# Optimization experiments

Hardware: AMD Instinct MI355X
Metric: run time of the kernel (lower is better)

Reference implementation:

```python
import jax, jax.numpy as jnp
import numpy as np
from jax.scipy.special import logsumexp

B, N1, N2, D = 32, 512, 512, 128
M_WARP = 256   # n_warp_fn_times
M_DISCR = 96   # n_warp_discr (warp-value grid per time step)
GAMMA = 0.1    # softmin temperature (soft relaxation of the hard-argmin GDTW DP)
BARRIER = 1e4  # soft penalty enforcing endpoint + local-gradient constraints


def setup_inputs() -> dict:
    key = jax.random.key(0)
    k1, k2, k3 = jax.random.split(key, 3)
    return {
        "signal1_features": jax.random.normal(k1, (B, N1, D), jnp.float32),
        "signal2_features": jax.random.normal(k2, (B, N2, D), jnp.float32),
        "reg_wt": jax.random.uniform(k3, (B,), jnp.float32, 0.1, 1.0),
        "glb_lb": jnp.zeros((B, M_WARP), jnp.float32),
        "glb_ub": jnp.ones((B, M_WARP), jnp.float32),
        "lcl_grad_ub": 2.0 * jnp.ones((B, 1), jnp.float32),
        "signal1_times": jnp.broadcast_to(jnp.linspace(0.0, 1.0, N1, dtype=jnp.float32)[None], (B, N1)),
        "signal2_times": jnp.broadcast_to(jnp.linspace(0.0, 1.0, N2, dtype=jnp.float32)[None], (B, N2)),
        "warp_fn_times": jnp.broadcast_to(jnp.linspace(0.0, 1.0, M_WARP, dtype=jnp.float32)[None], (B, M_WARP)),
    }


def _interp_uniform(feats, pos):
    """Linear interpolation of feats [b,n,d] at normalized positions pos in [0,1]."""
    b, n, d = feats.shape
    shp = pos.shape
    x = jnp.clip(pos, 0.0, 1.0) * (n - 1)
    i0 = jnp.clip(x.astype(jnp.int32), 0, n - 2)
    w = (x - i0.astype(x.dtype)).reshape(b, -1, 1)
    flat = i0.reshape(b, -1)
    f0 = jnp.take_along_axis(feats, flat[..., None], axis=1)
    f1 = jnp.take_along_axis(feats, flat[..., None] + 1, axis=1)
    return (f0 * (1.0 - w) + f1 * w).reshape(*shp, d)


def _softmin(x, axis):
    return -GAMMA * logsumexp(-x / GAMMA, axis=axis)


def _gdtw(s1f, s2f, reg_wt, glb_lb, glb_ub, lcl_grad_ub, t1, t2, tw):
    b, m = tw.shape
    T2 = jnp.max(t2, axis=1, keepdims=True)                       # [b,1]
    lb = glb_lb * T2
    ub = glb_ub * T2
    frac = jnp.linspace(0.0, 1.0, M_DISCR, dtype=tw.dtype)
    tau = lb[..., None] + (ub - lb)[..., None] * frac             # [b,m,M] candidate warp values
    s1_at = _interp_uniform(s1f, tw / jnp.max(t1, axis=1, keepdims=True))  # [b,m,d]
    s2_at = _interp_uniform(s2f, tau / T2[..., None])             # [b,m,M,d]
    diff = s1_at[:, :, None, :] - s2_at
    dtw_ = jnp.diff(tw, axis=1)                                   # [b,m-1]
    wts = 0.5 * jnp.concatenate([dtw_[:, :1], dtw_[:, 1:] + dtw_[:, :-1], dtw_[:, -1:]], axis=1)
    node = jnp.sum(diff * diff, axis=-1) * wts[..., None]         # [b,m,M] feature loss (p=2), trapezoid dt
    # endpoint constraints (subseq_enabled=False): phi(t0)=0, phi(tm)=T2
    node = node.at[:, 0].add(BARRIER * tau[:, 0] ** 2)
    node = node.at[:, -1].add(BARRIER * (tau[:, -1] - T2) ** 2)
    # transition costs: regularisation |phi' - 1|^2 dt + soft barriers for 0 <= phi' <= lcl_grad_ub
    slope = (tau[:, 1:, None, :] - tau[:, :-1, :, None]) / dtw_[:, :, None, None]  # [b,m-1,Mk,Mj]
    gub = lcl_grad_ub[:, :, None, None]
    pen = BARRIER * (jax.nn.relu(-slope) ** 2 + jax.nn.relu(slope - gub) ** 2)
    edge = reg_wt[:, None, None, None] * (slope - 1.0) ** 2 * dtw_[:, :, None, None] + pen
    edge_sc = jnp.moveaxis(edge, 1, 0)                            # [m-1,b,M,M]
    node_sc = jnp.moveaxis(node[:, 1:], 1, 0)                     # [m-1,b,M]

    def fwd_step(a, x):
        n_i, e_i = x
        a_new = n_i + _softmin(a[:, :, None] + e_i, axis=1)
        return a_new, a_new

    a0 = node[:, 0]
    _, alphas = jax.lax.scan(fwd_step, a0, (node_sc, edge_sc))
    alpha = jnp.concatenate([a0[None], alphas], axis=0)           # [m,b,M]

    def bwd_step(bn, x):
        n_ip1, e_i = x
        b_new = _softmin(e_i + (n_ip1 + bn)[:, None, :], axis=2)
        return b_new, b_new

    bT = jnp.zeros_like(a0)
    _, betas = jax.lax.scan(bwd_step, bT, (node_sc, edge_sc), reverse=True)
    beta = jnp.concatenate([betas, bT[None]], axis=0)             # [m,b,M]

    p = jax.nn.softmax(-(alpha + beta) / GAMMA, axis=-1)          # node marginals [m,b,M]
    return jnp.einsum('mbk,bmk->bm', p, tau)                      # expected warp values [b,m]


def reference(signal1_features, signal2_features, reg_wt, glb_lb, glb_ub, lcl_grad_ub, signal1_times, signal2_times, warp_fn_times):
    return _gdtw(signal1_features, signal2_features, reg_wt, glb_lb, glb_ub, lcl_grad_ub,
                 signal1_times, signal2_times, warp_fn_times)
```

## Files before the change

### kernel.cpp

```cpp
#include <hip/hip_runtime.h>

#define NB 32
#define N1 512
#define N2 512
#define DF 128
#define MW 256
#define KD 96
#define INVG 10.0f
#define GAM 0.1f
#define BARRIER 10000.0f

#define WS_NODE  0
#define WS_ABUF  (WS_NODE + NB*MW*KD)
#define WS_BBUF  (WS_ABUF + NB*MW*KD)

__device__ __forceinline__ bool feq(float a, float b) {
  return fabsf(a - b) <= 1e-4f * fmaxf(fabsf(a), fabsf(b)) + 1e-12f;
}

__device__ __forceinline__ float edgec(float s, float rdtv, float gub) {
  float d = s - 1.0f, ng = fminf(s, 0.f), ov = fmaxf(s - gub, 0.f);
  return rdtv*d*d + BARRIER*(ng*ng + ov*ov);
}

__device__ __forceinline__ float dpp_shr1(float x) {
  return __int_as_float(__builtin_amdgcn_update_dpp(
      0, __float_as_int(x), 0x138, 0xf, 0xf, true));
}
__device__ __forceinline__ float dpp_shl1(float x) {
  return __int_as_float(__builtin_amdgcn_update_dpp(
      0, __float_as_int(x), 0x130, 0xf, 0xf, true));
}

__global__ __launch_bounds__(256) void k1_node(const float* __restrict__ s1f,
                                               const float* __restrict__ s2f,
                                               const float* __restrict__ tw,
                                               const float* __restrict__ glb_lb,
                                               const float* __restrict__ glb_ub,
                                               const float* __restrict__ t1,
                                               const float* __restrict__ t2,
                                               float* __restrict__ ws) {
  const int id   = blockIdx.x;
  const int xcd  = id & 7;
  const int slot = id >> 3;
  const int b    = xcd + 8*(slot >> 4);
  const int mb   = slot & 15;
  const int t  = threadIdx.x;
  const int lane = t & 63;
  const int wv = t >> 6;
  __shared__ float s1L[16*132];
  __shared__ float s2L[96*132];
  __shared__ float ndt[16*99];
  __shared__ float wtsL[16], lbL[16], ubL[16];
  __shared__ int   matchL[16];
  __shared__ float redm[8];

  {
    float m1 = -1e30f, m2 = -1e30f;
    for (int i = t; i < N1; i += 256) m1 = fmaxf(m1, t1[b*N1+i]);
    for (int i = t; i < N2; i += 256) m2 = fmaxf(m2, t2[b*N2+i]);
    #pragma unroll
    for (int o = 32; o; o >>= 1) {
      m1 = fmaxf(m1, __shfl_down(m1, o));
      m2 = fmaxf(m2, __shfl_down(m2, o));
    }
    if (lane == 0) { redm[wv] = m1; redm[4+wv] = m2; }
  }
// ... 94 lines not shown
        }
      } else {
        const float lbm = lbL[mi], ubm = ubL[mi];
        int i0a[3]; float wa[3];
        #pragma unroll
        for (int j = 0; j < 3; j++) {
          int k = kt + 32*j;
          float tau = lbm + (ubm - lbm) * (float)k * (1.0f/95.0f);
          float x = fminf(fmaxf(tau / T2, 0.f), 1.f) * (float)(N2-1);
          int i0 = (int)x; i0 = max(0, min(i0, N2-2));
          i0a[j] = i0; wa[j] = x - (float)i0;
        }
        for (int d4 = 0; d4 < 32; d4++) {
          float4 s1v = s1L4[mi*33 + d4];
          #pragma unroll
          for (int j = 0; j < 3; j++) {
            float4 f0 = s2f4[(size_t)i0a[j]*32 + d4];
            float4 f1 = s2f4[(size_t)(i0a[j]+1)*32 + d4];
            float w = wa[j];
            float ax = f0.x + (f1.x - f0.x)*w, ay = f0.y + (f1.y - f0.y)*w;
            float az = f0.z + (f1.z - f0.z)*w, aw = f0.w + (f1.w - f0.w)*w;
            float dx = s1v.x - ax, dy = s1v.y - ay, dz = s1v.z - az, dw = s1v.w - aw;
            accp[j] += dx*dx + dy*dy + dz*dz + dw*dw;
          }
        }
      }
    }
  }
  {
    #pragma unroll
    for (int rr = 0; rr < 2; rr++) {
      const int mi = mi0 + rr;
      const int m = mb*16 + mi;
      const float wts = wtsL[mi];
      const float lbm = lbL[mi], ubm = ubL[mi];
      float* accp = rr ? acc1 : acc0;
      #pragma unroll
      for (int j = 0; j < 3; j++) {
        int k = kt + 32*j;
        float nodev = accp[j] * wts;
        float tau = lbm + (ubm - lbm) * (float)k * (1.0f/95.0f);
        if (m == 0)    nodev += BARRIER * tau * tau;
        if (m == MW-1) { float dd = tau - T2; nodev += BARRIER * dd * dd; }
        ndt[mi*99 + k] = nodev;
      }
    }
  }
  __syncthreads();
  float* nodeP = ws + WS_NODE + ((size_t)b*MW + mb*16)*KD;
  for (int idx = t; idx < 16*KD; idx += 256) {
    int mi2 = idx / KD, kv = idx - mi2*KD;
    nodeP[idx] = ndt[mi2*99 + kv];
  }
}

__global__ __launch_bounds__(512) void k2_out(const float* __restrict__ tw,
                                              const float* __restrict__ glb_lb,
                                              const float* __restrict__ glb_ub,
                                              const float* __restrict__ reg_wt,
                                              const float* __restrict__ gubp,
                                              const float* __restrict__ t2,
                                              float* __restrict__ ws,
                                              float* __restrict__ out) {
  const int b = blockIdx.x;
  const int t = threadIdx.x;
  const int wv = t >> 6;
  const int lane = t & 63;
  __shared__ float ndL[MW*KD];
  __shared__ float ndmL[MW];
  __shared__ float lbw[MW], ubw[MW], twv[MW];
  __shared__ float4 prmL[MW];
  __shared__ float dtL[MW];
  __shared__ float mir[2][KD];
  __shared__ float sred[32];
  __shared__ int skey[8];
  const float* __restrict__ nodeP = ws + WS_NODE + (size_t)b*MW*KD;

  {
    const float4* np4 = (const float4*)nodeP;
    float4* nl4 = (float4*)ndL;
    #pragma unroll
    for (int it = 0; it < (MW*KD/4)/512; it++)
      nl4[t + 512*it] = np4[t + 512*it];
  }
  {
    float m2 = -1e30f;
    for (int i = t; i < N2; i += 512) m2 = fmaxf(m2, t2[b*N2+i]);
    #pragma unroll
    for (int o = 32; o; o >>= 1) m2 = fmaxf(m2, __shfl_down(m2, o));
    if (lane == 0) sred[wv] = m2;
  }
  __syncthreads();
  float T2;
  {
    float v = sred[0];
    #pragma unroll
    for (int w = 1; w < 8; w++) v = fmaxf(v, sred[w]);
    T2 = v;
  }
  for (int i = t; i < MW; i += 512) {
    lbw[i] = glb_lb[b*MW+i]*T2;
    ubw[i] = glb_ub[b*MW+i]*T2;
    twv[i] = tw[b*MW+i];
  }
  const float r = reg_wt[b];
  const float gub = gubp[b];
  __syncthreads();

  const float lb0 = lbw[0], ub0 = ubw[0];
  const float g = (ub0 - lb0) * (1.0f/95.0f);
  bool keyok = true;
  float minE1 = 3e38f, minE2 = 3e38f, maxRdt = 0.f;
  for (int i = t; i < MW; i += 512)
    keyok = keyok && (lbw[i] == lb0) && (ubw[i] == ub0);
  for (int i = t; i < MW-1; i += 512) {
    float dtv = twv[i+1] - twv[i];
    if (!(dtv > 0.f)) keyok = false;
    else {
      float rdtv = r * dtv, sl = g / dtv;
      minE1 = fminf(minE1, fminf(edgec(sl, rdtv, gub), edgec(-sl, rdtv, gub)));
      minE2 = fminf(minE2, fminf(edgec(2.f*sl, rdtv, gub), edgec(-2.f*sl, rdtv, gub)));
      maxRdt = fmaxf(maxRdt, rdtv);
    }
  }

  const bool actS = t < KD;
  const int k = actS ? t : (KD-1);
  float P = 0.f, mx = 0.f;
  if (t < 128) {
    const bool hasn = actS && (k < KD-1);
    float P2 = 0.f;
    #pragma unroll 8
    for (int m = 0; m < MW; m++) {
      float a  = ndL[m*KD + k];
      float bq = hasn ? ndL[m*KD + k + 1] : a;
      P += a; P2 += bq;
      mx = fmaxf(mx, fabsf(P - P2));
    }
    if (!actS) mx = 0.f;
  }
  {
    float wmx = mx, wE1 = minE1, wE2 = minE2, wR = maxRdt;
    #pragma unroll
    for (int o = 32; o; o >>= 1) {
      wmx = fmaxf(wmx, __shfl_xor(wmx, o));
      wE1 = fminf(wE1, __shfl_xor(wE1, o));
      wE2 = fminf(wE2, __shfl_xor(wE2, o));
      wR  = fmaxf(wR,  __shfl_xor(wR,  o));
    }
    int ka = __all(keyok ? 1 : 0);
    if (lane == 0) {
      sred[wv*4+0] = wmx; sred[wv*4+1] = wE1;
      sred[wv*4+2] = wE2; sred[wv*4+3] = wR;
      skey[wv] = ka;
    }
  }
  __syncthreads();
  float MX, E1, E2, RD; int KAll;
  {
    float a0 = sred[0], a1 = sred[1], a2 = sred[2], a3 = sred[3];
    int kk2 = skey[0];
    #pragma unroll
    for (int w = 1; w < 8; w++) {
      a0 = fmaxf(a0, sred[w*4+0]);
      a1 = fminf(a1, sred[w*4+1]);
      a2 = fminf(a2, sred[w*4+2]);
      a3 = fmaxf(a3, sred[w*4+3]);
      kk2 = kk2 && skey[w];
    }
    MX = a0; E1 = a1; E2 = a2; RD = a3; KAll = kk2;
  }
  const bool ok = KAll &&
                  (2.0f*MX   <= E1 - RD - 3.0f) &&
                  (190.0f*MX <= E2 - RD - 3.0f);

  if (ok) {
    __syncthreads();
    float s = actS ? P : 3e38f;
    float mnv = s;
    #pragma unroll
    for (int o = 32; o; o >>= 1) mnv = fminf(mnv, __shfl_xor(mnv, o));
    if (lane == 0) sred[wv] = mnv;
    __syncthreads();
    float mn;
    {
      float v = sred[0];
      #pragma unroll
      for (int w = 1; w < 8; w++) v = fminf(v, sred[w]);
      mn = v;
    }
    float w = actS ? __expf((mn - P) * INVG) : 0.f;
    float num = w * (float)k, den = w;
    #pragma unroll
    for (int o = 32; o; o >>= 1) {
      num += __shfl_xor(num, o);
      den += __shfl_xor(den, o);
    }
    if (lane == 0) { sred[8+wv] = num; sred[16+wv] = den; }
    __syncthreads();
    float nsum, dsum;
    {
      float n0 = sred[8], d0 = sred[16];
      #pragma unroll
      for (int w2 = 1; w2 < 8; w2++) { n0 += sred[8+w2]; d0 += sred[16+w2]; }
      nsum = n0; dsum = d0;
    }
    const float q = (nsum / dsum) * (1.0f/95.0f);
    for (int m = t; m < MW; m += 512)
      out[b*MW + m] = lbw[m] + (ubw[m] - lbw[m]) * q;
    return;
  }

  {
    for (int i = t; i < MW-1; i += 512) {
      float4 p; p.x = lbw[i]; p.y = ubw[i]; p.z = lbw[i+1]; p.w = ubw[i+1];
      prmL[i] = p;
      dtL[i] = twv[i+1] - twv[i];
    }
    if (t < MW) {
      const float* rowp = &ndL[t*KD];
      float mnv = 3e38f;
      int c = lane;
      #pragma unroll 8
      for (int j = 0; j < KD; j++) {
        mnv = fminf(mnv, rowp[c]);
        c++; if (c >= KD) c -= KD;
      }
      ndmL[t] = mnv;
    }
    __syncthreads();

    if (t < 128) {
      const int dir = t >> 6;
      const bool act = lane < 48;
      const int k0i = 2*lane, k1i = 2*lane+1;
      const float frk0 = (float)k0i*(1.f/95.f), frk1 = (float)k1i*(1.f/95.f);
      float* __restrict__ outP = ws + (dir ? WS_BBUF : WS_ABUF) + (size_t)b*MW*KD;

      float a0 = 3e38f, a1 = 3e38f;
      {
        const int m0 = dir ? (MW-1) : 0;
        if (act) {
          a0 = ndL[m0*KD + k0i]; a1 = ndL[m0*KD + k1i];
          mir[dir][k0i] = a0; mir[dir][k1i] = a1;
          float2 o; o.x = dir ? 0.f : a0; o.y = dir ? 0.f : a1;
          *(float2*)&outP[(size_t)m0*KD + k0i] = o;
        }
      }
      float Blo;
      {
        float bl = act ? fminf(a0, a1) : 3e38f;
        #pragma unroll
        for (int o = 1; o < 64; o <<= 1) bl = fminf(bl, __shfl_xor(bl, o));
        Blo = bl;
      }
      float e00=3e38f,e0m=3e38f,e0p=3e38f,e10=3e38f,e1m=3e38f,e1p=3e38f;
      float eo0=3e38f, eo1=3e38f, eminmin=0.f;
      float cL1=__int_as_float(0x7fc00000), cU1=cL1, cL2=cL1, cU2=cL1, cdt=cL1;

      float4 pprm; float pdt; float pnd0=0.f, pnd1=0.f, pndm;
      {
        const int i0_ = dir ? (MW-2) : 0;
        pprm = prmL[i0_]; pdt = dtL[i0_];
        const int mn_ = dir ? i0_ : (i0_+1);
        if (act) { float2 v = *(const float2*)&ndL[mn_*KD + k0i]; pnd0=v.x; pnd1=v.y; }
        pndm = ndmL[mn_];
      }

      for (int step = 0; step < MW-1; step++) {
        const float L1=pprm.x, U1=pprm.y, L2=pprm.z, U2=pprm.w;
        const float dt = pdt;
        const float nd0=pnd0, nd1=pnd1, ndmn=pndm;
        {
          const int sn = (step+1 < MW-1) ? (step+1) : step;
          const int in_ = dir ? (MW-2-sn) : sn;
          pprm = prmL[in_]; pdt = dtL[in_];
          const int mn_ = dir ? in_ : (in_+1);
          if (act) { float2 v = *(const float2*)&ndL[mn_*KD + k0i]; pnd0=v.x; pnd1=v.y; }
          pndm = ndmL[mn_];
        }
        const bool kc = !(feq(L1,cL1)&&feq(U1,cU1)&&feq(L2,cL2)&&feq(U2,cU2)&&feq(dt,cdt));
        if (kc) {
          cL1=L1; cU1=U1; cL2=L2; cU2=U2; cdt=dt;
          float bl = act ? fminf(mir[dir][k0i], mir[dir][k1i]) : 3e38f;
          #pragma unroll
          for (int o = 1; o < 64; o <<= 1) bl = fminf(bl, __shfl_xor(bl, o));
          Blo = bl;
          const float invdt = 1.f/dt, rdt = r*dt;
          const float my0 = dir ? (L1+(U1-L1)*frk0) : (L2+(U2-L2)*frk0);
          const float my1 = dir ? (L1+(U1-L1)*frk1) : (L2+(U2-L2)*frk1);
          e00=3e38f; e0m=3e38f; e0p=3e38f; e10=3e38f; e1m=3e38f; e1p=3e38f;
          eo0=3e38f; eo1=3e38f;
          float emn = 3e38f;
          for (int j = 0; j < KD; j++) {
            const float frj = (float)j*(1.f/95.f);
            const float oth = dir ? (L2+(U2-L2)*frj) : (L1+(U1-L1)*frj);
            const float sl0 = (dir ? (oth-my0) : (my0-oth))*invdt;
            const float sl1 = (dir ? (oth-my1) : (my1-oth))*invdt;
            float d0=sl0-1.f, g0=fminf(sl0,0.f), v0=fmaxf(sl0-gub,0.f);
            float ej0 = rdt*d0*d0 + BARRIER*(g0*g0+v0*v0);
            float d1=sl1-1.f, g1=fminf(sl1,0.f), v1=fmaxf(sl1-gub,0.f);
            float ej1 = rdt*d1*d1 + BARRIER*(g1*g1+v1*v1);
            emn = fminf(emn, fminf(ej0, ej1));
            if      (j == k0i-1) e0m = ej0;
            else if (j == k0i)   e00 = ej0;
            else if (j == k0i+1) e0p = ej0;
            else                 eo0 = fminf(eo0, ej0);
            if      (j == k1i-1) e1m = ej1;
            else if (j == k1i)   e10 = ej1;
            else if (j == k1i+1) e1p = ej1;
            else                 eo1 = fminf(eo1, ej1);
          }
          if (!act) emn = 3e38f;
          #pragma unroll
          for (int o = 1; o < 64; o <<= 1) emn = fminf(emn, __shfl_xor(emn, o));
          eminmin = emn;
        }
        const float a1p = dpp_shr1(a1);
        const float a0n = dpp_shl1(a0);
        const float x0m = a1p + e0m;
        const float x00 = a0  + e00;
        const float x0p = a1  + e0p;
        const float x1m = a0  + e1m;
        const float x10 = a1  + e10;
        const float x1p = a0n + e1p;
        float mn0 = fminf(fminf(x0m, x00), x0p);
        float mn1 = fminf(fminf(x1m, x10), x1p);
        float sum0 = __expf((mn0-x0m)*INVG) + __expf((mn0-x00)*INVG) + __expf((mn0-x0p)*INVG);
        float sum1 = __expf((mn1-x1m)*INVG) + __expf((mn1-x10)*INVG) + __expf((mn1-x1p)*INVG);
        const bool bad = act && ((Blo + eo0 - mn0 < 8.7f) || (Blo + eo1 - mn1 < 8.7f));
        if (__any((int)bad)) {
          const float invdt = 1.f/dt, rdt = r*dt;
          const float my0 = dir ? (L1+(U1-L1)*frk0) : (L2+(U2-L2)*frk0);
          const float my1 = dir ? (L1+(U1-L1)*frk1) : (L2+(U2-L2)*frk1);
          mn0 = 3e38f; mn1 = 3e38f;
          for (int j = 0; j < KD; j++) {
            const float sj = mir[dir][j];
            const float frj = (float)j*(1.f/95.f);
            const float oth = dir ? (L2+(U2-L2)*frj) : (L1+(U1-L1)*frj);
            const float sl0 = (dir ? (oth-my0) : (my0-oth))*invdt;
            const float sl1 = (dir ? (oth-my1) : (my1-oth))*invdt;
            float d0=sl0-1.f, g0=fminf(sl0,0.f), v0=fmaxf(sl0-gub,0.f);
            float ej0 = rdt*d0*d0 + BARRIER*(g0*g0+v0*v0);
            float d1=sl1-1.f, g1=fminf(sl1,0.f), v1=fmaxf(sl1-gub,0.f);
            float ej1 = rdt*d1*d1 + BARRIER*(g1*g1+v1*v1);
            mn0 = fminf(mn0, fminf(sj + ej0, 3e38f));
            mn1 = fminf(mn1, fminf(sj + ej1, 3e38f));
          }
          sum0 = 0.f; sum1 = 0.f;
          for (int j = 0; j < KD; j++) {
            const float sj = mir[dir][j];
            const float frj = (float)j*(1.f/95.f);
            const float oth = dir ? (L2+(U2-L2)*frj) : (L1+(U1-L1)*frj);
            const float sl0 = (dir ? (oth-my0) : (my0-oth))*invdt;
            const float sl1 = (dir ? (oth-my1) : (my1-oth))*invdt;
            float d0=sl0-1.f, g0=fminf(sl0,0.f), v0=fmaxf(sl0-gub,0.f);
            float ej0 = rdt*d0*d0 + BARRIER*(g0*g0+v0*v0);
            float d1=sl1-1.f, g1=fminf(sl1,0.f), v1=fmaxf(sl1-gub,0.f);
            float ej1 = rdt*d1*d1 + BARRIER*(g1*g1+v1*v1);
            sum0 += __expf((mn0 - fminf(sj + ej0, 3e38f))*INVG);
            sum1 += __expf((mn1 - fminf(sj + ej1, 3e38f))*INVG);
          }
        }
        const float sv0 = mn0 - GAM*__logf(sum0);
        const float sv1 = mn1 - GAM*__logf(sum1);
        const float na0 = nd0 + sv0, na1 = nd1 + sv1;
        const int ic = dir ? (MW-2-step) : step;
        const int mnode = dir ? ic : (ic+1);
        if (act) {
          mir[dir][k0i] = na0; mir[dir][k1i] = na1;
          float2 o; o.x = dir ? sv0 : na0; o.y = dir ? sv1 : na1;
          *(float2*)&outP[(size_t)mnode*KD + k0i] = o;
        }
        a0 = act ? na0 : 3e38f;
        a1 = act ? na1 : 3e38f;
        Blo += eminmin + ndmn - 0.4575f;
      }
    }

    __threadfence_block();
    __syncthreads();
    const float* __restrict__ Ab = ws + WS_ABUF + (size_t)b*MW*KD;
    const float* __restrict__ Bb = ws + WS_BBUF + (size_t)b*MW*KD;
    for (int m = t; m < MW; m += 512) {
      const float4* Ab4 = (const float4*)&Ab[(size_t)m*KD];
      const float4* Bb4 = (const float4*)&Bb[(size_t)m*KD];
      float mnv = 3e38f;
      #pragma unroll 4
      for (int q = 0; q < KD/4; q++) {
        float4 av = Ab4[q], bv = Bb4[q];
        mnv = fminf(mnv, fminf(fminf(av.x+bv.x, av.y+bv.y),
                               fminf(av.z+bv.z, av.w+bv.w)));
      }
      float num = 0.f, den = 0.f;
      #pragma unroll 4
      for (int q = 0; q < KD/4; q++) {
        float4 av = Ab4[q], bv = Bb4[q];
        float w0 = __expf((mnv - (av.x+bv.x)) * INVG);
        float w1 = __expf((mnv - (av.y+bv.y)) * INVG);
        float w2 = __expf((mnv - (av.z+bv.z)) * INVG);
        float w3 = __expf((mnv - (av.w+bv.w)) * INVG);
        num += w0 * (float)(4*q+0); den += w0;
        num += w1 * (float)(4*q+1); den += w1;
        num += w2 * (float)(4*q+2); den += w2;
        num += w3 * (float)(4*q+3); den += w3;
      }
      out[b*MW + m] = lbw[m] + (ubw[m] - lbw[m]) * (num/den) * (1.0f/95.0f);
    }
  }
}

extern "C" void kernel_launch(void* const* d_in, const int* in_sizes, int n_in,
                              void* d_out, int out_size, void* d_ws, size_t ws_size,
                              hipStream_t stream) {
  const float* s1f    = (const float*)d_in[0];
  const float* s2f    = (const float*)d_in[1];
  const float* regw   = (const float*)d_in[2];
  const float* glb_lb = (const float*)d_in[3];
  const float* glb_ub = (const float*)d_in[4];
  const float* gubp   = (const float*)d_in[5];
  const float* t1     = (const float*)d_in[6];
  const float* t2     = (const float*)d_in[7];
  const float* twp    = (const float*)d_in[8];
  float* ws  = (float*)d_ws;
  float* out = (float*)d_out;

  k1_node<<<512, 256, 0, stream>>>(s1f, s2f, twp, glb_lb, glb_ub, t1, t2, ws);
  k2_out<<<NB, 512, 0, stream>>>(twp, glb_lb, glb_ub, regw, gubp, t2, ws, out);
}
```

Before: 104.9 us.

## Overlap node streaming, fast-path scan and DP recursion via double-buffered chunks

Result: slower. 242.1 us (+130.8%).

```diff
diff --git a/kernel.cpp b/kernel.cpp
--- a/kernel.cpp
+++ b/kernel.cpp
@@ -13,6 +13,7 @@
 #define WS_NODE  0
 #define WS_ABUF  (WS_NODE + NB*MW*KD)
 #define WS_BBUF  (WS_ABUF + NB*MW*KD)
+#define WS_NDM   (WS_BBUF + NB*MW*KD)
 
 __device__ __forceinline__ bool feq(float a, float b) {
   return fabsf(a - b) <= 1e-4f * fmaxf(fabsf(a), fabsf(b)) + 1e-12f;
@@ -213,6 +214,12 @@
     int mi2 = idx / KD, kv = idx - mi2*KD;
     nodeP[idx] = ndt[mi2*99 + kv];
   }
+  if (t < 16) {
+    const float* rp = &ndt[t*99];
+    float mn = 3e38f;
+    for (int kk = 0; kk < KD; kk++) mn = fminf(mn, rp[kk]);
+    ws[WS_NDM + (size_t)b*MW + mb*16 + t] = mn;
+  }
 }
 
 __global__ __launch_bounds__(512) void k2_out(const float* __restrict__ tw,
@@ -227,7 +234,8 @@
   const int t = threadIdx.x;
   const int wv = t >> 6;
   const int lane = t & 63;
-  __shared__ float ndL[MW*KD];
+  __shared__ float FB0[32*KD], FB1[32*KD];
+  __shared__ float BB0[32*KD], BB1[32*KD];
   __shared__ float ndmL[MW];
   __shared__ float lbw[MW], ubw[MW], twv[MW];
   __shared__ float4 prmL[MW];
@@ -236,14 +244,8 @@
   __shared__ float sred[32];
   __shared__ int skey[8];
   const float* __restrict__ nodeP = ws + WS_NODE + (size_t)b*MW*KD;
-
-  {
-    const float4* np4 = (const float4*)nodeP;
-    float4* nl4 = (float4*)ndL;
-    #pragma unroll
-    for (int it = 0; it < (MW*KD/4)/512; it++)
-      nl4[t + 512*it] = np4[t + 512*it];
-  }
+  const float4* np4 = (const float4*)nodeP;
+
   {
     float m2 = -1e30f;
     for (int i = t; i < N2; i += 512) m2 = fmaxf(m2, t2[b*N2+i]);
@@ -263,10 +265,21 @@
     lbw[i] = glb_lb[b*MW+i]*T2;
     ubw[i] = glb_ub[b*MW+i]*T2;
     twv[i] = tw[b*MW+i];
+    ndmL[i] = ws[WS_NDM + (size_t)b*MW + i];
+  }
+  for (int e = t; e < 768; e += 512) {
+    int j = e/24, c4 = e - j*24;
+    ((float4*)FB0)[j*24+c4] = np4[(1+j)*24 + c4];
+    ((float4*)BB0)[j*24+c4] = np4[(254-j)*24 + c4];
   }
   const float r = reg_wt[b];
   const float gub = gubp[b];
   __syncthreads();
+  for (int i = t; i < MW-1; i += 512) {
+    float4 p; p.x = lbw[i]; p.y = ubw[i]; p.z = lbw[i+1]; p.w = ubw[i+1];
+    prmL[i] = p;
+    dtL[i] = twv[i+1] - twv[i];
+  }
 
   const float lb0 = lbw[0], ub0 = ubw[0];
   const float g = (ub0 - lb0) * (1.0f/95.0f);
@@ -285,160 +298,72 @@
     }
   }
 
-  const bool actS = t < KD;
-  const int k = actS ? t : (KD-1);
-  float P = 0.f, mx = 0.f;
+  const bool isScan = (t >= 128 && t < 224);
+  const int k = isScan ? (t - 128) : (KD-1);
+  const bool hasn = isScan && (k < KD-1);
+  float P = 0.f, P2 = 0.f, mx = 0.f;
+  if (isScan) {
+    float a = nodeP[k];
+    float bq = hasn ? nodeP[k+1] : a;
+    P = a; P2 = bq; mx = fabsf(P - P2);
+  }
+
+  const int dir = t >> 6;
+  const bool act = (t < 128) && (lane < 48);
+  const int k0i = 2*lane, k1i = 2*lane+1;
+  const float frk0 = (float)k0i*(1.f/95.f), frk1 = (float)k1i*(1.f/95.f);
+  float* __restrict__ outP = ws + (dir ? WS_BBUF : WS_ABUF) + (size_t)b*MW*KD;
+  float a0 = 3e38f, a1 = 3e38f;
+  float Blo = 3e38f;
+  float e00=3e38f,e0m=3e38f,e0p=3e38f,e10=3e38f,e1m=3e38f,e1p=3e38f;
+  float eo0=3e38f, eo1=3e38f, eminmin=0.f;
+  float cL1=__int_as_float(0x7fc00000), cU1=cL1, cL2=cL1, cU2=cL1, cdt=cL1;
+  float4 pprm; float pdt=1.f; float pnd0=0.f, pnd1=0.f, pndm=0.f;
+  pprm.x=0.f; pprm.y=0.f; pprm.z=0.f; pprm.w=0.f;
+
   if (t < 128) {
-    const bool hasn = actS && (k < KD-1);
-    float P2 = 0.f;
-    #pragma unroll 8
-    for (int m = 0; m < MW; m++) {
-      float a  = ndL[m*KD + k];
-      float bq = hasn ? ndL[m*KD + k + 1] : a;
-      P += a; P2 += bq;
-      mx = fmaxf(mx, fabsf(P - P2));
-    }
-    if (!actS) mx = 0.f;
-  }
-  {
-    float wmx = mx, wE1 = minE1, wE2 = minE2, wR = maxRdt;
-    #pragma unroll
-    for (int o = 32; o; o >>= 1) {
-      wmx = fmaxf(wmx, __shfl_xor(wmx, o));
-      wE1 = fminf(wE1, __shfl_xor(wE1, o));
-      wE2 = fminf(wE2, __shfl_xor(wE2, o));
-      wR  = fmaxf(wR,  __shfl_xor(wR,  o));
-    }
-    int ka = __all(keyok ? 1 : 0);
-    if (lane == 0) {
-      sred[wv*4+0] = wmx; sred[wv*4+1] = wE1;
-      sred[wv*4+2] = wE2; sred[wv*4+3] = wR;
-      skey[wv] = ka;
-    }
-  }
-  __syncthreads();
-  float MX, E1, E2, RD; int KAll;
-  {
-    float a0 = sred[0], a1 = sred[1], a2 = sred[2], a3 = sred[3];
-    int kk2 = skey[0];
-    #pragma unroll
-    for (int w = 1; w < 8; w++) {
-      a0 = fmaxf(a0, sred[w*4+0]);
-      a1 = fminf(a1, sred[w*4+1]);
-      a2 = fminf(a2, sred[w*4+2]);
-      a3 = fmaxf(a3, sred[w*4+3]);
-      kk2 = kk2 && skey[w];
-    }
-    MX = a0; E1 = a1; E2 = a2; RD = a3; KAll = kk2;
-  }
-  const bool ok = KAll &&
-                  (2.0f*MX   <= E1 - RD - 3.0f) &&
-                  (190.0f*MX <= E2 - RD - 3.0f);
-
-  if (ok) {
-    __syncthreads();
-    float s = actS ? P : 3e38f;
-    float mnv = s;
-    #pragma unroll
-    for (int o = 32; o; o >>= 1) mnv = fminf(mnv, __shfl_xor(mnv, o));
-    if (lane == 0) sred[wv] = mnv;
-    __syncthreads();
-    float mn;
-    {
-      float v = sred[0];
-      #pragma unroll
-      for (int w = 1; w < 8; w++) v = fminf(v, sred[w]);
-      mn = v;
-    }
-    float w = actS ? __expf((mn - P) * INVG) : 0.f;
-    float num = w * (float)k, den = w;
-    #pragma unroll
-    for (int o = 32; o; o >>= 1) {
-      num += __shfl_xor(num, o);
-      den += __shfl_xor(den, o);
-    }
-    if (lane == 0) { sred[8+wv] = num; sred[16+wv] = den; }
-    __syncthreads();
-    float nsum, dsum;
-    {
-      float n0 = sred[8], d0 = sred[16];
-      #pragma unroll
-      for (int w2 = 1; w2 < 8; w2++) { n0 += sred[8+w2]; d0 += sred[16+w2]; }
-      nsum = n0; dsum = d0;
-    }
-    const float q = (nsum / dsum) * (1.0f/95.0f);
-    for (int m = t; m < MW; m += 512)
-      out[b*MW + m] = lbw[m] + (ubw[m] - lbw[m]) * q;
-    return;
-  }
-
-  {
-    for (int i = t; i < MW-1; i += 512) {
-      float4 p; p.x = lbw[i]; p.y = ubw[i]; p.z = lbw[i+1]; p.w = ubw[i+1];
-      prmL[i] = p;
-      dtL[i] = twv[i+1] - twv[i];
-    }
-    if (t < MW) {
-      const float* rowp = &ndL[t*KD];
-      float mnv = 3e38f;
-      int c = lane;
-      #pragma unroll 8
-      for (int j = 0; j < KD; j++) {
-        mnv = fminf(mnv, rowp[c]);
-        c++; if (c >= KD) c -= KD;
-      }
-      ndmL[t] = mnv;
-    }
-    __syncthreads();
-
+    const int m0 = dir ? (MW-1) : 0;
+    if (act) {
+      float2 v = *(const float2*)&nodeP[(size_t)m0*KD + k0i];
+      a0 = v.x; a1 = v.y;
+      mir[dir][k0i] = a0; mir[dir][k1i] = a1;
+      float2 o; o.x = dir ? 0.f : a0; o.y = dir ? 0.f : a1;
+      *(float2*)&outP[(size_t)m0*KD + k0i] = o;
+    }
+    float bl = act ? fminf(a0, a1) : 3e38f;
+    #pragma unroll
+    for (int o = 1; o < 64; o <<= 1) bl = fminf(bl, __shfl_xor(bl, o));
+    Blo = bl;
+  }
+  __syncthreads();
+
+  #pragma unroll 1
+  for (int s = 0; s < 8; s++) {
+    float* fb_cur = (s & 1) ? FB1 : FB0;
+    float* bb_cur = (s & 1) ? BB1 : BB0;
     if (t < 128) {
-      const int dir = t >> 6;
-      const bool act = lane < 48;
-      const int k0i = 2*lane, k1i = 2*lane+1;
-      const float frk0 = (float)k0i*(1.f/95.f), frk1 = (float)k1i*(1.f/95.f);
-      float* __restrict__ outP = ws + (dir ? WS_BBUF : WS_ABUF) + (size_t)b*MW*KD;
-
-      float a0 = 3e38f, a1 = 3e38f;
+      const int sigma = 32*s;
+      const int last = (s == 7) ? 30 : 31;
       {
-        const int m0 = dir ? (MW-1) : 0;
-        if (act) {
-          a0 = ndL[m0*KD + k0i]; a1 = ndL[m0*KD + k1i];
-          mir[dir][k0i] = a0; mir[dir][k1i] = a1;
-          float2 o; o.x = dir ? 0.f : a0; o.y = dir ? 0.f : a1;
-          *(float2*)&outP[(size_t)m0*KD + k0i] = o;
-        }
-      }
-      float Blo;
-      {
-        float bl = act ? fminf(a0, a1) : 3e38f;
-        #pragma unroll
-        for (int o = 1; o < 64; o <<= 1) bl = fminf(bl, __shfl_xor(bl, o));
-        Blo = bl;
-      }
-      float e00=3e38f,e0m=3e38f,e0p=3e38f,e10=3e38f,e1m=3e38f,e1p=3e38f;
-      float eo0=3e38f, eo1=3e38f, eminmin=0.f;
-      float cL1=__int_as_float(0x7fc00000), cU1=cL1, cL2=cL1, cU2=cL1, cdt=cL1;
-
-      float4 pprm; float pdt; float pnd0=0.f, pnd1=0.f, pndm;
-      {
-        const int i0_ = dir ? (MW-2) : 0;
-        pprm = prmL[i0_]; pdt = dtL[i0_];
-        const int mn_ = dir ? i0_ : (i0_+1);
-        if (act) { float2 v = *(const float2*)&ndL[mn_*KD + k0i]; pnd0=v.x; pnd1=v.y; }
-        pndm = ndmL[mn_];
-      }
-
-      for (int step = 0; step < MW-1; step++) {
+        const int in0 = dir ? (254 - sigma) : sigma;
+        pprm = prmL[in0]; pdt = dtL[in0];
+        pndm = ndmL[dir ? (254 - sigma) : (sigma + 1)];
+        const float* cb = dir ? bb_cur : fb_cur;
+        if (act) { float2 v = *(const float2*)&cb[k0i]; pnd0 = v.x; pnd1 = v.y; }
+      }
+      #pragma unroll 1
+      for (int i = 0; i <= last; i++) {
+        const int step = sigma + i;
         const float L1=pprm.x, U1=pprm.y, L2=pprm.z, U2=pprm.w;
         const float dt = pdt;
         const float nd0=pnd0, nd1=pnd1, ndmn=pndm;
-        {
-          const int sn = (step+1 < MW-1) ? (step+1) : step;
-          const int in_ = dir ? (MW-2-sn) : sn;
+        if (i < last) {
+          const int sn = step + 1;
+          const int in_ = dir ? (254 - sn) : sn;
           pprm = prmL[in_]; pdt = dtL[in_];
-          const int mn_ = dir ? in_ : (in_+1);
-          if (act) { float2 v = *(const float2*)&ndL[mn_*KD + k0i]; pnd0=v.x; pnd1=v.y; }
-          pndm = ndmL[mn_];
+          pndm = ndmL[dir ? (254 - sn) : (sn + 1)];
+          const float* cb = dir ? bb_cur : fb_cur;
+          if (act) { float2 v = *(const float2*)&cb[(i+1)*KD + k0i]; pnd0 = v.x; pnd1 = v.y; }
         }
         const bool kc = !(feq(L1,cL1)&&feq(U1,cU1)&&feq(L2,cL2)&&feq(U2,cU2)&&feq(dt,cdt));
         if (kc) {
@@ -537,10 +462,108 @@
         a1 = act ? na1 : 3e38f;
         Blo += eminmin + ndmn - 0.4575f;
       }
-    }
-
-    __threadfence_block();
+    } else if (isScan) {
+      const float* fb = fb_cur;
+      const int jmax = (s == 7) ? 31 : 32;
+      for (int j = 0; j < jmax; j++) {
+        float a = fb[j*KD + k];
+        float bq = hasn ? fb[j*KD + k + 1] : a;
+        P += a; P2 += bq;
+        mx = fmaxf(mx, fabsf(P - P2));
+      }
+    } else {
+      if (s < 7) {
+        const int sp = s + 1;
+        float* fbn = (sp & 1) ? FB1 : FB0;
+        float* bbn = (sp & 1) ? BB1 : BB0;
+        const int u = t - 224;
+        for (int e = u; e < 768; e += 288) {
+          int j = e/24, c4 = e - j*24;
+          int row = 32*sp + 1 + j; if (row > 255) row = 255;
+          ((float4*)fbn)[j*24+c4] = np4[row*24 + c4];
+          int row2 = 254 - 32*sp - j; if (row2 < 0) row2 = 0;
+          ((float4*)bbn)[j*24+c4] = np4[row2*24 + c4];
+        }
+      }
+    }
     __syncthreads();
+  }
+
+  {
+    float wmx = mx, wE1 = minE1, wE2 = minE2, wR = maxRdt;
+    #pragma unroll
+    for (int o = 32; o; o >>= 1) {
+      wmx = fmaxf(wmx, __shfl_xor(wmx, o));
+      wE1 = fminf(wE1, __shfl_xor(wE1, o));
+      wE2 = fminf(wE2, __shfl_xor(wE2, o));
+      wR  = fmaxf(wR,  __shfl_xor(wR,  o));
+    }
+    int ka = __all(keyok ? 1 : 0);
+    if (lane == 0) {
+      sred[wv*4+0] = wmx; sred[wv*4+1] = wE1;
+      sred[wv*4+2] = wE2; sred[wv*4+3] = wR;
+      skey[wv] = ka;
+    }
+  }
+  __syncthreads();
+  float MX, E1, E2, RD; int KAll;
+  {
+    float a0r = sred[0], a1r = sred[1], a2r = sred[2], a3r = sred[3];
+    int kk2 = skey[0];
+    #pragma unroll
+    for (int w = 1; w < 8; w++) {
+      a0r = fmaxf(a0r, sred[w*4+0]);
+      a1r = fminf(a1r, sred[w*4+1]);
+      a2r = fminf(a2r, sred[w*4+2]);
+      a3r = fmaxf(a3r, sred[w*4+3]);
+      kk2 = kk2 && skey[w];
+    }
+    MX = a0r; E1 = a1r; E2 = a2r; RD = a3r; KAll = kk2;
+  }
+  const bool ok = KAll &&
+                  (2.0f*MX   <= E1 - RD - 3.0f) &&
+                  (190.0f*MX <= E2 - RD - 3.0f);
+
+  if (ok) {
+    __syncthreads();
+    float sP = isScan ? P : 3e38f;
+    float mnv = sP;
+    #pragma unroll
+    for (int o = 32; o; o >>= 1) mnv = fminf(mnv, __shfl_xor(mnv, o));
+    if (lane == 0) sred[wv] = mnv;
+    __syncthreads();
+    float mn;
+    {
+      float v = sred[0];
+      #pragma unroll
+      for (int w = 1; w < 8; w++) v = fminf(v, sred[w]);
+      mn = v;
+    }
+    float w = isScan ? __expf((mn - P) * INVG) : 0.f;
+    float num = w * (float)k, den = w;
+    #pragma unroll
+    for (int o = 32; o; o >>= 1) {
+      num += __shfl_xor(num, o);
+      den += __shfl_xor(den, o);
+    }
+    if (lane == 0) { sred[8+wv] = num; sred[16+wv] = den; }
+    __syncthreads();
+    float nsum, dsum;
+    {
+      float n0 = sred[8], d0 = sred[16];
+      #pragma unroll
+      for (int w2 = 1; w2 < 8; w2++) { n0 += sred[8+w2]; d0 += sred[16+w2]; }
+      nsum = n0; dsum = d0;
+    }
+    const float q = (nsum / dsum) * (1.0f/95.0f);
+    for (int m = t; m < MW; m += 512)
+      out[b*MW + m] = lbw[m] + (ubw[m] - lbw[m]) * q;
+    return;
+  }
+
+  __threadfence_block();
+  __syncthreads();
+  {
     const float* __restrict__ Ab = ws + WS_ABUF + (size_t)b*MW*KD;
     const float* __restrict__ Bb = ws + WS_BBUF + (size_t)b*MW*KD;
     for (int m = t; m < MW; m += 512) {
```

## Run DP scans speculatively in parallel with fast-path check; precompute row minima in k1

Applied to the files above, without the earlier changes.

After: 232.3 us. 2.21x slower.

```diff
diff --git a/kernel.cpp b/kernel.cpp
--- a/kernel.cpp
+++ b/kernel.cpp
@@ -13,6 +13,7 @@
 #define WS_NODE  0
 #define WS_ABUF  (WS_NODE + NB*MW*KD)
 #define WS_BBUF  (WS_ABUF + NB*MW*KD)
+#define WS_NDM   (WS_BBUF + NB*MW*KD)
 
 __device__ __forceinline__ bool feq(float a, float b) {
   return fabsf(a - b) <= 1e-4f * fmaxf(fabsf(a), fabsf(b)) + 1e-12f;
@@ -213,6 +214,12 @@
     int mi2 = idx / KD, kv = idx - mi2*KD;
     nodeP[idx] = ndt[mi2*99 + kv];
   }
+  if (t < 16) {
+    const float* rp = &ndt[t*99];
+    float mn = 3e38f;
+    for (int kk = 0; kk < KD; kk++) mn = fminf(mn, rp[kk]);
+    ws[WS_NDM + (size_t)b*MW + mb*16 + t] = mn;
+  }
 }
 
 __global__ __launch_bounds__(512) void k2_out(const float* __restrict__ tw,
@@ -263,43 +270,202 @@
     lbw[i] = glb_lb[b*MW+i]*T2;
     ubw[i] = glb_ub[b*MW+i]*T2;
     twv[i] = tw[b*MW+i];
+    ndmL[i] = ws[WS_NDM + (size_t)b*MW + i];
   }
   const float r = reg_wt[b];
   const float gub = gubp[b];
   __syncthreads();
-
-  const float lb0 = lbw[0], ub0 = ubw[0];
-  const float g = (ub0 - lb0) * (1.0f/95.0f);
+  if (t < 128) {
+    for (int i = t; i < MW-1; i += 128) {
+      float4 p; p.x = lbw[i]; p.y = ubw[i]; p.z = lbw[i+1]; p.w = ubw[i+1];
+      prmL[i] = p;
+      dtL[i] = twv[i+1] - twv[i];
+    }
+  }
+  __syncthreads();
+
+  const bool isScan = (t >= 128 && t < 224);
+  const int k = isScan ? (t - 128) : (KD-1);
+  float P = 0.f, mx = 0.f;
   bool keyok = true;
   float minE1 = 3e38f, minE2 = 3e38f, maxRdt = 0.f;
-  for (int i = t; i < MW; i += 512)
-    keyok = keyok && (lbw[i] == lb0) && (ubw[i] == ub0);
-  for (int i = t; i < MW-1; i += 512) {
-    float dtv = twv[i+1] - twv[i];
-    if (!(dtv > 0.f)) keyok = false;
-    else {
-      float rdtv = r * dtv, sl = g / dtv;
-      minE1 = fminf(minE1, fminf(edgec(sl, rdtv, gub), edgec(-sl, rdtv, gub)));
-      minE2 = fminf(minE2, fminf(edgec(2.f*sl, rdtv, gub), edgec(-2.f*sl, rdtv, gub)));
-      maxRdt = fmaxf(maxRdt, rdtv);
-    }
-  }
-
-  const bool actS = t < KD;
-  const int k = actS ? t : (KD-1);
-  float P = 0.f, mx = 0.f;
-  if (t < 128) {
-    const bool hasn = actS && (k < KD-1);
-    float P2 = 0.f;
-    #pragma unroll 8
-    for (int m = 0; m < MW; m++) {
-      float a  = ndL[m*KD + k];
-      float bq = hasn ? ndL[m*KD + k + 1] : a;
-      P += a; P2 += bq;
-      mx = fmaxf(mx, fabsf(P - P2));
-    }
-    if (!actS) mx = 0.f;
-  }
+
+  if (t >= 128) {
+    const float lb0 = lbw[0], ub0 = ubw[0];
+    const float g = (ub0 - lb0) * (1.0f/95.0f);
+    for (int i = t-128; i < MW; i += 384)
+      keyok = keyok && (lbw[i] == lb0) && (ubw[i] == ub0);
+    for (int i = t-128; i < MW-1; i += 384) {
+      float dtv = twv[i+1] - twv[i];
+      if (!(dtv > 0.f)) keyok = false;
+      else {
+        float rdtv = r * dtv, sl = g / dtv;
+        minE1 = fminf(minE1, fminf(edgec(sl, rdtv, gub), edgec(-sl, rdtv, gub)));
+        minE2 = fminf(minE2, fminf(edgec(2.f*sl, rdtv, gub), edgec(-2.f*sl, rdtv, gub)));
+        maxRdt = fmaxf(maxRdt, rdtv);
+      }
+    }
+    if (isScan) {
+      const bool hasn = (k < KD-1);
+      float P2 = 0.f;
+      #pragma unroll 8
+      for (int m = 0; m < MW; m++) {
+        float a  = ndL[m*KD + k];
+        float bq = hasn ? ndL[m*KD + k + 1] : a;
+        P += a; P2 += bq;
+        mx = fmaxf(mx, fabsf(P - P2));
+      }
+    }
+  } else {
+    const int dir = t >> 6;
+    const bool act = lane < 48;
+    const int k0i = 2*lane, k1i = 2*lane+1;
+    const float frk0 = (float)k0i*(1.f/95.f), frk1 = (float)k1i*(1.f/95.f);
+    float* __restrict__ outP = ws + (dir ? WS_BBUF : WS_ABUF) + (size_t)b*MW*KD;
+
+    float a0 = 3e38f, a1 = 3e38f;
+    {
+      const int m0 = dir ? (MW-1) : 0;
+      if (act) {
+        a0 = ndL[m0*KD + k0i]; a1 = ndL[m0*KD + k1i];
+        mir[dir][k0i] = a0; mir[dir][k1i] = a1;
+        float2 o; o.x = dir ? 0.f : a0; o.y = dir ? 0.f : a1;
+        *(float2*)&outP[(size_t)m0*KD + k0i] = o;
+      }
+    }
+    float Blo;
+    {
+      float bl = act ? fminf(a0, a1) : 3e38f;
+      #pragma unroll
+      for (int o = 1; o < 64; o <<= 1) bl = fminf(bl, __shfl_xor(bl, o));
+      Blo = bl;
+    }
+    float e00=3e38f,e0m=3e38f,e0p=3e38f,e10=3e38f,e1m=3e38f,e1p=3e38f;
+    float eo0=3e38f, eo1=3e38f, eminmin=0.f;
+    float cL1=__int_as_float(0x7fc00000), cU1=cL1, cL2=cL1, cU2=cL1, cdt=cL1;
+
+    float4 pprm; float pdt; float pnd0=0.f, pnd1=0.f, pndm;
+    {
+      const int i0_ = dir ? (MW-2) : 0;
+      pprm = prmL[i0_]; pdt = dtL[i0_];
+      const int mn_ = dir ? i0_ : (i0_+1);
+      if (act) { float2 v = *(const float2*)&ndL[mn_*KD + k0i]; pnd0=v.x; pnd1=v.y; }
+      pndm = ndmL[mn_];
+    }
+
+    for (int step = 0; step < MW-1; step++) {
+      const float L1=pprm.x, U1=pprm.y, L2=pprm.z, U2=pprm.w;
+      const float dt = pdt;
+      const float nd0=pnd0, nd1=pnd1, ndmn=pndm;
+      {
+        const int sn = (step+1 < MW-1) ? (step+1) : step;
+        const int in_ = dir ? (MW-2-sn) : sn;
+        pprm = prmL[in_]; pdt = dtL[in_];
+        const int mn_ = dir ? in_ : (in_+1);
+        if (act) { float2 v = *(const float2*)&ndL[mn_*KD + k0i]; pnd0=v.x; pnd1=v.y; }
+        pndm = ndmL[mn_];
+      }
+      const bool kc = !(feq(L1,cL1)&&feq(U1,cU1)&&feq(L2,cL2)&&feq(U2,cU2)&&feq(dt,cdt));
+      if (kc) {
+        cL1=L1; cU1=U1; cL2=L2; cU2=U2; cdt=dt;
+        float bl = act ? fminf(mir[dir][k0i], mir[dir][k1i]) : 3e38f;
+        #pragma unroll
+        for (int o = 1; o < 64; o <<= 1) bl = fminf(bl, __shfl_xor(bl, o));
+        Blo = bl;
+        const float invdt = 1.f/dt, rdt = r*dt;
+        const float my0 = dir ? (L1+(U1-L1)*frk0) : (L2+(U2-L2)*frk0);
+        const float my1 = dir ? (L1+(U1-L1)*frk1) : (L2+(U2-L2)*frk1);
+        e00=3e38f; e0m=3e38f; e0p=3e38f; e10=3e38f; e1m=3e38f; e1p=3e38f;
+        eo0=3e38f; eo1=3e38f;
+        float emn = 3e38f;
+        for (int j = 0; j < KD; j++) {
+          const float frj = (float)j*(1.f/95.f);
+          const float oth = dir ? (L2+(U2-L2)*frj) : (L1+(U1-L1)*frj);
+          const float sl0 = (dir ? (oth-my0) : (my0-oth))*invdt;
+          const float sl1 = (dir ? (oth-my1) : (my1-oth))*invdt;
+          float d0=sl0-1.f, g0=fminf(sl0,0.f), v0=fmaxf(sl0-gub,0.f);
+          float ej0 = rdt*d0*d0 + BARRIER*(g0*g0+v0*v0);
+          float d1=sl1-1.f, g1=fminf(sl1,0.f), v1=fmaxf(sl1-gub,0.f);
+          float ej1 = rdt*d1*d1 + BARRIER*(g1*g1+v1*v1);
+          emn = fminf(emn, fminf(ej0, ej1));
+          if      (j == k0i-1) e0m = ej0;
+          else if (j == k0i)   e00 = ej0;
+          else if (j == k0i+1) e0p = ej0;
+          else                 eo0 = fminf(eo0, ej0);
+          if      (j == k1i-1) e1m = ej1;
+          else if (j == k1i)   e10 = ej1;
+          else if (j == k1i+1) e1p = ej1;
+          else                 eo1 = fminf(eo1, ej1);
+        }
+        if (!act) emn = 3e38f;
+        #pragma unroll
+        for (int o = 1; o < 64; o <<= 1) emn = fminf(emn, __shfl_xor(emn, o));
+        eminmin = emn;
+      }
+      const float a1p = dpp_shr1(a1);
+      const float a0n = dpp_shl1(a0);
+      const float x0m = a1p + e0m;
+      const float x00 = a0  + e00;
+      const float x0p = a1  + e0p;
+      const float x1m = a0  + e1m;
+      const float x10 = a1  + e10;
+      const float x1p = a0n + e1p;
+      float mn0 = fminf(fminf(x0m, x00), x0p);
+      float mn1 = fminf(fminf(x1m, x10), x1p);
+      float sum0 = __expf((mn0-x0m)*INVG) + __expf((mn0-x00)*INVG) + __expf((mn0-x0p)*INVG);
+      float sum1 = __expf((mn1-x1m)*INVG) + __expf((mn1-x10)*INVG) + __expf((mn1-x1p)*INVG);
+      const bool bad = act && ((Blo + eo0 - mn0 < 8.7f) || (Blo + eo1 - mn1 < 8.7f));
+      if (__any((int)bad)) {
+        const float invdt = 1.f/dt, rdt = r*dt;
+        const float my0 = dir ? (L1+(U1-L1)*frk0) : (L2+(U2-L2)*frk0);
+        const float my1 = dir ? (L1+(U1-L1)*frk1) : (L2+(U2-L2)*frk1);
+        mn0 = 3e38f; mn1 = 3e38f;
+        for (int j = 0; j < KD; j++) {
+          const float sj = mir[dir][j];
+          const float frj = (float)j*(1.f/95.f);
+          const float oth = dir ? (L2+(U2-L2)*frj) : (L1+(U1-L1)*frj);
+          const float sl0 = (dir ? (oth-my0) : (my0-oth))*invdt;
+          const float sl1 = (dir ? (oth-my1) : (my1-oth))*invdt;
+          float d0=sl0-1.f, g0=fminf(sl0,0.f), v0=fmaxf(sl0-gub,0.f);
+          float ej0 = rdt*d0*d0 + BARRIER*(g0*g0+v0*v0);
+          float d1=sl1-1.f, g1=fminf(sl1,0.f), v1=fmaxf(sl1-gub,0.f);
+          float ej1 = rdt*d1*d1 + BARRIER*(g1*g1+v1*v1);
+          mn0 = fminf(mn0, fminf(sj + ej0, 3e38f));
+          mn1 = fminf(mn1, fminf(sj + ej1, 3e38f));
+        }
+        sum0 = 0.f; sum1 = 0.f;
+        for (int j = 0; j < KD; j++) {
+          const float sj = mir[dir][j];
+          const float frj = (float)j*(1.f/95.f);
+          const float oth = dir ? (L2+(U2-L2)*frj) : (L1+(U1-L1)*frj);
+          const float sl0 = (dir ? (oth-my0) : (my0-oth))*invdt;
+          const float sl1 = (dir ? (oth-my1) : (my1-oth))*invdt;
+          float d0=sl0-1.f, g0=fminf(sl0,0.f), v0=fmaxf(sl0-gub,0.f);
+          float ej0 = rdt*d0*d0 + BARRIER*(g0*g0+v0*v0);
+          float d1=sl1-1.f, g1=fminf(sl1,0.f), v1=fmaxf(sl1-gub,0.f);
+          float ej1 = rdt*d1*d1 + BARRIER*(g1*g1+v1*v1);
+          sum0 += __expf((mn0 - fminf(sj + ej0, 3e38f))*INVG);
+          sum1 += __expf((mn1 - fminf(sj + ej1, 3e38f))*INVG);
+        }
+      }
+      const float sv0 = mn0 - GAM*__logf(sum0);
+      const float sv1 = mn1 - GAM*__logf(sum1);
+      const float na0 = nd0 + sv0, na1 = nd1 + sv1;
+      const int ic = dir ? (MW-2-step) : step;
+      const int mnode = dir ? ic : (ic+1);
+      if (act) {
+        mir[dir][k0i] = na0; mir[dir][k1i] = na1;
+        float2 o; o.x = dir ? sv0 : na0; o.y = dir ? sv1 : na1;
+        *(float2*)&outP[(size_t)mnode*KD + k0i] = o;
+      }
+      a0 = act ? na0 : 3e38f;
+      a1 = act ? na1 : 3e38f;
+      Blo += eminmin + ndmn - 0.4575f;
+    }
+  }
+
+  __threadfence_block();
+  __syncthreads();
   {
     float wmx = mx, wE1 = minE1, wE2 = minE2, wR = maxRdt;
     #pragma unroll
@@ -319,17 +485,17 @@
   __syncthreads();
   float MX, E1, E2, RD; int KAll;
   {
-    float a0 = sred[0], a1 = sred[1], a2 = sred[2], a3 = sred[3];
+    float a0r = sred[0], a1r = sred[1], a2r = sred[2], a3r = sred[3];
     int kk2 = skey[0];
     #pragma unroll
     for (int w = 1; w < 8; w++) {
-      a0 = fmaxf(a0, sred[w*4+0]);
-      a1 = fminf(a1, sred[w*4+1]);
-      a2 = fminf(a2, sred[w*4+2]);
-      a3 = fmaxf(a3, sred[w*4+3]);
+      a0r = fmaxf(a0r, sred[w*4+0]);
+      a1r = fminf(a1r, sred[w*4+1]);
+      a2r = fminf(a2r, sred[w*4+2]);
+      a3r = fmaxf(a3r, sred[w*4+3]);
       kk2 = kk2 && skey[w];
     }
-    MX = a0; E1 = a1; E2 = a2; RD = a3; KAll = kk2;
+    MX = a0r; E1 = a1r; E2 = a2r; RD = a3r; KAll = kk2;
   }
   const bool ok = KAll &&
                   (2.0f*MX   <= E1 - RD - 3.0f) &&
@@ -337,8 +503,8 @@
 
   if (ok) {
     __syncthreads();
-    float s = actS ? P : 3e38f;
-    float mnv = s;
+    float sP = isScan ? P : 3e38f;
+    float mnv = sP;
     #pragma unroll
     for (int o = 32; o; o >>= 1) mnv = fminf(mnv, __shfl_xor(mnv, o));
     if (lane == 0) sred[wv] = mnv;
@@ -350,7 +516,7 @@
       for (int w = 1; w < 8; w++) v = fminf(v, sred[w]);
       mn = v;
     }
-    float w = actS ? __expf((mn - P) * INVG) : 0.f;
+    float w = isScan ? __expf((mn - P) * INVG) : 0.f;
     float num = w * (float)k, den = w;
     #pragma unroll
     for (int o = 32; o; o >>= 1) {
@@ -373,174 +539,6 @@
   }
 
   {
-    for (int i = t; i < MW-1; i += 512) {
-      float4 p; p.x = lbw[i]; p.y = ubw[i]; p.z = lbw[i+1]; p.w = ubw[i+1];
-      prmL[i] = p;
-      dtL[i] = twv[i+1] - twv[i];
-    }
-    if (t < MW) {
-      const float* rowp = &ndL[t*KD];
-      float mnv = 3e38f;
-      int c = lane;
-      #pragma unroll 8
-      for (int j = 0; j < KD; j++) {
-        mnv = fminf(mnv, rowp[c]);
-        c++; if (c >= KD) c -= KD;
-      }
-      ndmL[t] = mnv;
-    }
-    __syncthreads();
-
-    if (t < 128) {
-      const int dir = t >> 6;
-      const bool act = lane < 48;
-      const int k0i = 2*lane, k1i = 2*lane+1;
-      const float frk0 = (float)k0i*(1.f/95.f), frk1 = (float)k1i*(1.f/95.f);
-      float* __restrict__ outP = ws + (dir ? WS_BBUF : WS_ABUF) + (size_t)b*MW*KD;
-
-      float a0 = 3e38f, a1 = 3e38f;
-      {
-        const int m0 = dir ? (MW-1) : 0;
-        if (act) {
-          a0 = ndL[m0*KD + k0i]; a1 = ndL[m0*KD + k1i];
-          mir[dir][k0i] = a0; mir[dir][k1i] = a1;
-          float2 o; o.x = dir ? 0.f : a0; o.y = dir ? 0.f : a1;
-          *(float2*)&outP[(size_t)m0*KD + k0i] = o;
-        }
-      }
-      float Blo;
-      {
-        float bl = act ? fminf(a0, a1) : 3e38f;
-        #pragma unroll
-        for (int o = 1; o < 64; o <<= 1) bl = fminf(bl, __shfl_xor(bl, o));
-        Blo = bl;
-      }
-      float e00=3e38f,e0m=3e38f,e0p=3e38f,e10=3e38f,e1m=3e38f,e1p=3e38f;
-      float eo0=3e38f, eo1=3e38f, eminmin=0.f;
-      float cL1=__int_as_float(0x7fc00000), cU1=cL1, cL2=cL1, cU2=cL1, cdt=cL1;
-
-      float4 pprm; float pdt; float pnd0=0.f, pnd1=0.f, pndm;
-      {
-        const int i0_ = dir ? (MW-2) : 0;
-        pprm = prmL[i0_]; pdt = dtL[i0_];
-        const int mn_ = dir ? i0_ : (i0_+1);
-        if (act) { float2 v = *(const float2*)&ndL[mn_*KD + k0i]; pnd0=v.x; pnd1=v.y; }
-        pndm = ndmL[mn_];
-      }
-
-      for (int step = 0; step < MW-1; step++) {
-        const float L1=pprm.x, U1=pprm.y, L2=pprm.z, U2=pprm.w;
-        const float dt = pdt;
-        const float nd0=pnd0, nd1=pnd1, ndmn=pndm;
-        {
-          const int sn = (step+1 < MW-1) ? (step+1) : step;
-          const int in_ = dir ? (MW-2-sn) : sn;
-          pprm = prmL[in_]; pdt = dtL[in_];
-          const int mn_ = dir ? in_ : (in_+1);
-          if (act) { float2 v = *(const float2*)&ndL[mn_*KD + k0i]; pnd0=v.x; pnd1=v.y; }
-          pndm = ndmL[mn_];
-        }
-        const bool kc = !(feq(L1,cL1)&&feq(U1,cU1)&&feq(L2,cL2)&&feq(U2,cU2)&&feq(dt,cdt));
-        if (kc) {
-          cL1=L1; cU1=U1; cL2=L2; cU2=U2; cdt=dt;
-          float bl = act ? fminf(mir[dir][k0i], mir[dir][k1i]) : 3e38f;
-          #pragma unroll
-          for (int o = 1; o < 64; o <<= 1) bl = fminf(bl, __shfl_xor(bl, o));
-          Blo = bl;
-          const float invdt = 1.f/dt, rdt = r*dt;
-          const float my0 = dir ? (L1+(U1-L1)*frk0) : (L2+(U2-L2)*frk0);
-          const float my1 = dir ? (L1+(U1-L1)*frk1) : (L2+(U2-L2)*frk1);
-          e00=3e38f; e0m=3e38f; e0p=3e38f; e10=3e38f; e1m=3e38f; e1p=3e38f;
-          eo0=3e38f; eo1=3e38f;
-          float emn = 3e38f;
-          for (int j = 0; j < KD; j++) {
-            const float frj = (float)j*(1.f/95.f);
-            const float oth = dir ? (L2+(U2-L2)*frj) : (L1+(U1-L1)*frj);
-            const float sl0 = (dir ? (oth-my0) : (my0-oth))*invdt;
-            const float sl1 = (dir ? (oth-my1) : (my1-oth))*invdt;
-            float d0=sl0-1.f, g0=fminf(sl0,0.f), v0=fmaxf(sl0-gub,0.f);
-            float ej0 = rdt*d0*d0 + BARRIER*(g0*g0+v0*v0);
-            float d1=sl1-1.f, g1=fminf(sl1,0.f), v1=fmaxf(sl1-gub,0.f);
-            float ej1 = rdt*d1*d1 + BARRIER*(g1*g1+v1*v1);
-            emn = fminf(emn, fminf(ej0, ej1));
-            if      (j == k0i-1) e0m = ej0;
-            else if (j == k0i)   e00 = ej0;
-            else if (j == k0i+1) e0p = ej0;
-            else                 eo0 = fminf(eo0, ej0);
-            if      (j == k1i-1) e1m = ej1;
-            else if (j == k1i)   e10 = ej1;
-            else if (j == k1i+1) e1p = ej1;
-            else                 eo1 = fminf(eo1, ej1);
-          }
-          if (!act) emn = 3e38f;
-          #pragma unroll
-          for (int o = 1; o < 64; o <<= 1) emn = fminf(emn, __shfl_xor(emn, o));
-          eminmin = emn;
-        }
-        const float a1p = dpp_shr1(a1);
-        const float a0n = dpp_shl1(a0);
-        const float x0m = a1p + e0m;
-        const float x00 = a0  + e00;
-        const float x0p = a1  + e0p;
-        const float x1m = a0  + e1m;
-        const float x10 = a1  + e10;
-        const float x1p = a0n + e1p;
-        float mn0 = fminf(fminf(x0m, x00), x0p);
-        float mn1 = fminf(fminf(x1m, x10), x1p);
-        float sum0 = __expf((mn0-x0m)*INVG) + __expf((mn0-x00)*INVG) + __expf((mn0-x0p)*INVG);
-        float sum1 = __expf((mn1-x1m)*INVG) + __expf((mn1-x10)*INVG) + __expf((mn1-x1p)*INVG);
-        const bool bad = act && ((Blo + eo0 - mn0 < 8.7f) || (Blo + eo1 - mn1 < 8.7f));
-        if (__any((int)bad)) {
-          const float invdt = 1.f/dt, rdt = r*dt;
-          const float my0 = dir ? (L1+(U1-L1)*frk0) : (L2+(U2-L2)*frk0);
-          const float my1 = dir ? (L1+(U1-L1)*frk1) : (L2+(U2-L2)*frk1);
-          mn0 = 3e38f; mn1 = 3e38f;
-          for (int j = 0; j < KD; j++) {
-            const float sj = mir[dir][j];
-            const float frj = (float)j*(1.f/95.f);
-            const float oth = dir ? (L2+(U2-L2)*frj) : (L1+(U1-L1)*frj);
-            const float sl0 = (dir ? (oth-my0) : (my0-oth))*invdt;
-            const float sl1 = (dir ? (oth-my1) : (my1-oth))*invdt;
-            float d0=sl0-1.f, g0=fminf(sl0,0.f), v0=fmaxf(sl0-gub,0.f);
-            float ej0 = rdt*d0*d0 + BARRIER*(g0*g0+v0*v0);
-            float d1=sl1-1.f, g1=fminf(sl1,0.f), v1=fmaxf(sl1-gub,0.f);
-            float ej1 = rdt*d1*d1 + BARRIER*(g1*g1+v1*v1);
-            mn0 = fminf(mn0, fminf(sj + ej0, 3e38f));
-            mn1 = fminf(mn1, fminf(sj + ej1, 3e38f));
-          }
-          sum0 = 0.f; sum1 = 0.f;
-          for (int j = 0; j < KD; j++) {
-            const float sj = mir[dir][j];
-            const float frj = (float)j*(1.f/95.f);
-            const float oth = dir ? (L2+(U2-L2)*frj) : (L1+(U1-L1)*frj);
-            const float sl0 = (dir ? (oth-my0) : (my0-oth))*invdt;
-            const float sl1 = (dir ? (oth-my1) : (my1-oth))*invdt;
-            float d0=sl0-1.f, g0=fminf(sl0,0.f), v0=fmaxf(sl0-gub,0.f);
-            float ej0 = rdt*d0*d0 + BARRIER*(g0*g0+v0*v0);
-            float d1=sl1-1.f, g1=fminf(sl1,0.f), v1=fmaxf(sl1-gub,0.f);
-            float ej1 = rdt*d1*d1 + BARRIER*(g1*g1+v1*v1);
-            sum0 += __expf((mn0 - fminf(sj + ej0, 3e38f))*INVG);
-            sum1 += __expf((mn1 - fminf(sj + ej1, 3e38f))*INVG);
-          }
-        }
-        const float sv0 = mn0 - GAM*__logf(sum0);
-        const float sv1 = mn1 - GAM*__logf(sum1);
-        const float na0 = nd0 + sv0, na1 = nd1 + sv1;
-        const int ic = dir ? (MW-2-step) : step;
-        const int mnode = dir ? ic : (ic+1);
-        if (act) {
-          mir[dir][k0i] = na0; mir[dir][k1i] = na1;
-          float2 o; o.x = dir ? sv0 : na0; o.y = dir ? sv1 : na1;
-          *(float2*)&outP[(size_t)mnode*KD + k0i] = o;
-        }
-        a0 = act ? na0 : 3e38f;
-        a1 = act ? na1 : 3e38f;
-        Blo += eminmin + ndmn - 0.4575f;
-      }
-    }
-
-    __threadfence_block();
-    __syncthreads();
     const float* __restrict__ Ab = ws + WS_ABUF + (size_t)b*MW*KD;
     const float* __restrict__ Bb = ws + WS_BBUF + (size_t)b*MW*KD;
     for (int m = t; m < MW; m += 512) {
```
